# Kernel optimization log

Hardware: AMD Instinct MI355X
Metric: run time of the kernel (lower is better)

Reference implementation:

```python
import jax, jax.numpy as jnp
import numpy as np

P = 7      # local_patch_size
H = 6      # heads
DH = 30    # dim_head


def setup_inputs() -> dict:
    key = jax.random.key(0)
    ks = jax.random.split(key, 5)
    b, dim, L = 16, 180, 14336
    inner = H * DH  # 180
    fmap = jax.random.normal(ks[0], (b, dim, L), dtype=jnp.float32)
    Wq = jax.random.normal(ks[1], (inner, dim), dtype=jnp.float32) * 0.05
    Wkv = jax.random.normal(ks[2], (2 * inner, dim), dtype=jnp.float32) * 0.05
    Wo = jax.random.normal(ks[3], (dim, inner), dtype=jnp.float32) * 0.05
    bo = jax.random.normal(ks[4], (dim,), dtype=jnp.float32) * 0.05
    return {"fmap": fmap, "Wq": Wq, "Wkv": Wkv, "Wo": Wo, "bo": bo}


def reference(fmap, Wq, Wkv, Wo, bo):
    b, c, L = fmap.shape
    l = L // P
    scale = DH ** -0.5
    # 'b c (l p) -> b c l p' windows
    x = fmap.reshape(b, c, l, P)
    # pointwise (kernel-1) conv projections
    q = jnp.einsum('ec,bclp->belp', Wq, x)
    kv = jnp.einsum('ec,bclp->belp', Wkv, x)
    k, v = jnp.split(kv, 2, axis=1)

    def split_heads(t):
        # (b, h*d, l, p) -> (b, l, h, p, d)
        return t.reshape(b, H, DH, l, P).transpose(0, 3, 1, 4, 2)

    q, k, v = map(split_heads, (q, k, v))
    dots = jnp.einsum('blhid,blhjd->blhij', q, k) * scale  # per-window 7x7 scores
    attn = jax.nn.softmax(dots, axis=-1)
    out = jnp.einsum('blhij,blhjd->blhid', attn, v)  # (b, l, h, p, d)
    # '(b l h) p d -> b (h d) (l p)'
    out = out.transpose(0, 2, 4, 1, 3).reshape(b, H * DH, l * P)
    return jnp.einsum('oe,bel->bol', Wo, out) + bo[None, :, None]
```

## Files before the change

kernel.cpp:

```cpp
#include <hip/hip_runtime.h>
#include <stdint.h>

namespace {

constexpr int DIM  = 180;
constexpr int LL   = 14336;
constexpr int B    = 16;
constexpr int T    = 56;
constexpr int NCH  = 256;
constexpr int EQKV = 540;
constexpr int EPAD = 192;

constexpr int QT_STRIDE = 584;
constexpr int XS_STRIDE = 200;
constexpr int QT_U16  = T * QT_STRIDE;
constexpr int XS_U16  = 32 * XS_STRIDE;
constexpr int LDS_U16 = QT_U16 + XS_U16 + 544;

typedef __attribute__((ext_vector_type(8))) short bf16x8;
typedef __attribute__((ext_vector_type(4))) float f32x4;

union Frag { bf16x8 v; uint32_t u[4]; unsigned short s[8]; };

__device__ __forceinline__ unsigned short f2b(float f) {
  uint32_t u = __builtin_bit_cast(uint32_t, f);
  u = (u + 0x7fffu + ((u >> 16) & 1u)) >> 16;
  return (unsigned short)u;
}
__device__ __forceinline__ uint32_t pack2(float lo, float hi) {
  return (uint32_t)f2b(lo) | ((uint32_t)f2b(hi) << 16);
}
__device__ __forceinline__ float blo(uint32_t u) { return __builtin_bit_cast(float, u << 16); }
__device__ __forceinline__ float bhi(uint32_t u) { return __builtin_bit_cast(float, u & 0xffff0000u); }
__device__ __forceinline__ f32x4 zero4() { f32x4 z = {0.f,0.f,0.f,0.f}; return z; }
__device__ __forceinline__ bf16x8 zfrag() {
  Frag f; f.u[0]=f.u[1]=f.u[2]=f.u[3]=0u; return f.v;
}

}

__global__ __launch_bounds__(1024) void la_prep(
    const float* __restrict__ Wq, const float* __restrict__ Wkv,
    const float* __restrict__ Wo, unsigned short* __restrict__ wqkv_b,
    unsigned short* __restrict__ wo_b) {
  const int idx = (int)(blockIdx.x * 1024 + threadIdx.x);
  if (idx < EQKV * EPAD) {
    const int e = idx / EPAD, c = idx - e * EPAD;
    float v = 0.f;
    if (c < DIM) v = (e < DIM) ? Wq[e * DIM + c] : Wkv[(size_t)(e - DIM) * DIM + c];
    wqkv_b[idx] = f2b(v);
  } else {
    const int k = idx - EQKV * EPAD;
    if (k < DIM * EPAD) {
      const int o = k / EPAD, cc = k - o * EPAD;
      const int h = cc >> 5, d = cc & 31;
      float v = 0.f;
      if (d < 30) v = Wo[o * DIM + h * 30 + d];
      wo_b[k] = f2b(v);
    }
  }
}

__global__ __launch_bounds__(512, 4) void la_main(
    const float* __restrict__ fmap, const unsigned short* __restrict__ wqkv,
    const unsigned short* __restrict__ wo_b, const float* __restrict__ bo,
    float* __restrict__ out) {
  __shared__ unsigned short lds[LDS_U16];
  unsigned short* qt  = lds;
  unsigned short* xs  = lds + QT_U16;
  unsigned short* lut = xs + XS_U16;

  const int tid  = (int)threadIdx.x;
  const int wave = tid >> 6;
  const int lane = tid & 63;
  const int l15  = lane & 15;
  const int g    = lane >> 4;

  const int bi    = (int)blockIdx.x;
  const int b     = bi >> 8;
  const int chunk = bi & 255;
  const int t0    = chunk * T;

  for (int e = tid; e < EQKV; e += 512) {
    const int part = (e >= 360) ? 2 : ((e >= DIM) ? 1 : 0);
    const int rr = e - part * DIM;
    const int h = rr / 30;
    const int d = rr - h * 30;
    lut[e] = (unsigned short)(part * EPAD + h * 32 + d);
  }

#pragma unroll
  for (int ph = 0; ph < 2; ++ph) {
    const int tb = ph * 32;
    __syncthreads();
#pragma unroll
    for (int it = 0; it < 3; ++it) {
      const int idx = tid + it * 512;
      const int c  = idx >> 3;
      const int tl = (idx & 7) * 4;
      float4 v = {0.f, 0.f, 0.f, 0.f};
      if (c < DIM && (tb + tl) < T)
        v = *(const float4*)(fmap + (size_t)(b * DIM + c) * LL + t0 + tb + tl);
      unsigned short* xr = xs + tl * XS_STRIDE + c;
      xr[0 * XS_STRIDE] = f2b(v.x);
      xr[1 * XS_STRIDE] = f2b(v.y);
      xr[2 * XS_STRIDE] = f2b(v.z);
      xr[3 * XS_STRIDE] = f2b(v.w);
    }
    __syncthreads();
    for (int mt = wave; mt < 36; mt += 8) {
      const int e_a = mt * 16 + l15;
      f32x4 acc0 = zero4(), acc1 = zero4();
#pragma unroll
      for (int ks = 0; ks < 6; ++ks) {
        const int c0 = ks * 32 + g * 8;
        const bf16x8 a = (e_a < EQKV)
            ? *(const bf16x8*)(wqkv + (size_t)e_a * EPAD + c0) : zfrag();
        const bf16x8 b0 = *(const bf16x8*)(xs + l15 * XS_STRIDE + c0);
        const bf16x8 b1 = *(const bf16x8*)(xs + (16 + l15) * XS_STRIDE + c0);
        acc0 = __builtin_amdgcn_mfma_f32_16x16x32_bf16(a, b0, acc0, 0, 0, 0);
        acc1 = __builtin_amdgcn_mfma_f32_16x16x32_bf16(a, b1, acc1, 0, 0, 0);
      }
      const int e0 = mt * 16 + g * 4;
#pragma unroll
      for (int nt = 0; nt < 2; ++nt) {
        const f32x4 A = nt ? acc1 : acc0;
        const int t = tb + nt * 16 + l15;
        if (t < T) {
          unsigned short* qrow = qt + t * QT_STRIDE;
          if (e0 + 0 < EQKV) qrow[lut[e0 + 0]] = f2b(A[0]);
          if (e0 + 1 < EQKV) qrow[lut[e0 + 1]] = f2b(A[1]);
          if (e0 + 2 < EQKV) qrow[lut[e0 + 2]] = f2b(A[2]);
          if (e0 + 3 < EQKV) qrow[lut[e0 + 3]] = f2b(A[3]);
        }
      }
    }
  }
  __syncthreads();

  if (tid < 336) {
    const float scale = 0.18257418583505536f;
    const int w   = tid / 42;
    const int rem = tid - w * 42;
    const int h   = rem / 7;
    const int i   = rem - h * 7;
    const int ti  = w * 7 + i;
    const uint32_t* qrow = (const uint32_t*)(qt + ti * QT_STRIDE + h * 32);
    const unsigned short* kbase = qt + (w * 7) * QT_STRIDE + EPAD + h * 32;
    float dots[7];
#pragma unroll
    for (int j = 0; j < 7; ++j) dots[j] = 0.f;
#pragma unroll
    for (int dp = 0; dp < 15; ++dp) {
      const uint32_t qu = qrow[dp];
      const float q0 = blo(qu), q1 = bhi(qu);
#pragma unroll
      for (int j = 0; j < 7; ++j) {
        const uint32_t ku = *(const uint32_t*)(kbase + j * QT_STRIDE + dp * 2);
        dots[j] += q0 * blo(ku);
        dots[j] += q1 * bhi(ku);
      }
    }
    float mx = dots[0];
#pragma unroll
    for (int j = 1; j < 7; ++j) mx = fmaxf(mx, dots[j]);
    float aw[7];
    float s = 0.f;
#pragma unroll
    for (int j = 0; j < 7; ++j) {
      const float pj = __expf(scale * (dots[j] - mx));
      aw[j] = pj; s += pj;
    }
    const float inv = 1.f / s;
#pragma unroll
    for (int j = 0; j < 7; ++j) aw[j] *= inv;
    const unsigned short* vbase = qt + (w * 7) * QT_STRIDE + 2 * EPAD + h * 32;
    uint32_t* orow = (uint32_t*)(qt + ti * QT_STRIDE + h * 32);
#pragma unroll
    for (int dp = 0; dp < 15; ++dp) {
      float o0 = 0.f, o1 = 0.f;
#pragma unroll
      for (int j = 0; j < 7; ++j) {
        const uint32_t vu = *(const uint32_t*)(vbase + j * QT_STRIDE + dp * 2);
        o0 += aw[j] * blo(vu);
        o1 += aw[j] * bhi(vu);
      }
      orow[dp] = pack2(o0, o1);
    }
    orow[15] = 0u;
  }
  __syncthreads();

  for (int p = wave; p < 48; p += 8) {
    const int m = p >> 2;
    const int n = p & 3;
    const int o_a  = m * 16 + l15;
    const int tcol = n * 16 + l15;
    const int trd  = (tcol < T) ? tcol : (T - 1);
    f32x4 acc = zero4();
#pragma unroll
    for (int ks = 0; ks < 6; ++ks) {
      const int c0 = ks * 32 + g * 8;
      const bf16x8 a = (o_a < DIM)
          ? *(const bf16x8*)(wo_b + (size_t)o_a * EPAD + c0) : zfrag();
      const bf16x8 bf = *(const bf16x8*)(qt + trd * QT_STRIDE + c0);
      acc = __builtin_amdgcn_mfma_f32_16x16x32_bf16(a, bf, acc, 0, 0, 0);
    }
    if (tcol < T) {
#pragma unroll
      for (int r = 0; r < 4; ++r) {
        const int o = m * 16 + g * 4 + r;
        if (o < DIM)
          out[(size_t)(b * DIM + o) * LL + t0 + tcol] = acc[r] + bo[o];
      }
    }
  }
}

extern "C" void kernel_launch(void* const* d_in, const int* in_sizes, int n_in,
                              void* d_out, int out_size, void* d_ws, size_t ws_size,
                              hipStream_t stream) {
  const float* fmap = (const float*)d_in[0];
  const float* Wq   = (const float*)d_in[1];
  const float* Wkv  = (const float*)d_in[2];
  const float* Wo   = (const float*)d_in[3];
  const float* bo   = (const float*)d_in[4];
  float* o = (float*)d_out;

  unsigned short* wqkv_b = (unsigned short*)d_ws;
  unsigned short* wo_b   = wqkv_b + EQKV * EPAD;

  const int prep_elems = EQKV * EPAD + DIM * EPAD;
  hipLaunchKernelGGL(la_prep, dim3((prep_elems + 1023) / 1024), dim3(1024), 0,
                     stream, Wq, Wkv, Wo, wqkv_b, wo_b);
  hipLaunchKernelGGL(la_main, dim3(B * NCH), dim3(512), 0, stream,
                     fmap, wqkv_b, wo_b, bo, o);
}
```

Baseline: 401.3 us.

## Halve token tile and load activations straight into MFMA register fragments

The token tile per block drops from 56 to 28, which doubles the grid. Each lane now gathers its fmap column straight into bf16 MFMA B-fragments held in registers, so the LDS staging buffer, its extra barriers and the LUT are gone. The head/dim index is computed arithmetically instead. This shrinks LDS so more blocks fit per CU (launch bounds raised to 6), but the per-lane fmap reads are strided by a full row rather than coalesced float4 loads, and each weight matrix fragment is reused over only 28 tokens.

Result: slower. 576.5 us (+43.7%).

```diff
diff --git a/kernel.cpp b/kernel.cpp
--- a/kernel.cpp
+++ b/kernel.cpp
@@ -6,16 +6,12 @@
 constexpr int DIM  = 180;
 constexpr int LL   = 14336;
 constexpr int B    = 16;
-constexpr int T    = 56;
-constexpr int NCH  = 256;
+constexpr int T    = 28;
+constexpr int NCH  = 512;
 constexpr int EQKV = 540;
 constexpr int EPAD = 192;
 
 constexpr int QT_STRIDE = 584;
-constexpr int XS_STRIDE = 200;
-constexpr int QT_U16  = T * QT_STRIDE;
-constexpr int XS_U16  = 32 * XS_STRIDE;
-constexpr int LDS_U16 = QT_U16 + XS_U16 + 544;
 
 typedef __attribute__((ext_vector_type(8))) short bf16x8;
 typedef __attribute__((ext_vector_type(4))) float f32x4;
@@ -61,14 +57,11 @@
   }
 }
 
-__global__ __launch_bounds__(512, 4) void la_main(
+__global__ __launch_bounds__(512, 6) void la_main(
     const float* __restrict__ fmap, const unsigned short* __restrict__ wqkv,
     const unsigned short* __restrict__ wo_b, const float* __restrict__ bo,
     float* __restrict__ out) {
-  __shared__ unsigned short lds[LDS_U16];
-  unsigned short* qt  = lds;
-  unsigned short* xs  = lds + QT_U16;
-  unsigned short* lut = xs + XS_U16;
+  __shared__ __align__(16) unsigned short qt[T * QT_STRIDE];
 
   const int tid  = (int)threadIdx.x;
   const int wave = tid >> 6;
@@ -77,68 +70,61 @@
   const int g    = lane >> 4;
 
   const int bi    = (int)blockIdx.x;
-  const int b     = bi >> 8;
-  const int chunk = bi & 255;
+  const int b     = bi >> 9;
+  const int chunk = bi & 511;
   const int t0    = chunk * T;
 
-  for (int e = tid; e < EQKV; e += 512) {
-    const int part = (e >= 360) ? 2 : ((e >= DIM) ? 1 : 0);
-    const int rr = e - part * DIM;
-    const int h = rr / 30;
-    const int d = rr - h * 30;
-    lut[e] = (unsigned short)(part * EPAD + h * 32 + d);
-  }
-
-#pragma unroll
-  for (int ph = 0; ph < 2; ++ph) {
-    const int tb = ph * 32;
-    __syncthreads();
-#pragma unroll
-    for (int it = 0; it < 3; ++it) {
-      const int idx = tid + it * 512;
-      const int c  = idx >> 3;
-      const int tl = (idx & 7) * 4;
-      float4 v = {0.f, 0.f, 0.f, 0.f};
-      if (c < DIM && (tb + tl) < T)
-        v = *(const float4*)(fmap + (size_t)(b * DIM + c) * LL + t0 + tb + tl);
-      unsigned short* xr = xs + tl * XS_STRIDE + c;
-      xr[0 * XS_STRIDE] = f2b(v.x);
-      xr[1 * XS_STRIDE] = f2b(v.y);
-      xr[2 * XS_STRIDE] = f2b(v.z);
-      xr[3 * XS_STRIDE] = f2b(v.w);
-    }
-    __syncthreads();
-    for (int mt = wave; mt < 36; mt += 8) {
-      const int e_a = mt * 16 + l15;
-      f32x4 acc0 = zero4(), acc1 = zero4();
-#pragma unroll
-      for (int ks = 0; ks < 6; ++ks) {
-        const int c0 = ks * 32 + g * 8;
-        const bf16x8 a = (e_a < EQKV)
-            ? *(const bf16x8*)(wqkv + (size_t)e_a * EPAD + c0) : zfrag();
-        const bf16x8 b0 = *(const bf16x8*)(xs + l15 * XS_STRIDE + c0);
-        const bf16x8 b1 = *(const bf16x8*)(xs + (16 + l15) * XS_STRIDE + c0);
-        acc0 = __builtin_amdgcn_mfma_f32_16x16x32_bf16(a, b0, acc0, 0, 0, 0);
-        acc1 = __builtin_amdgcn_mfma_f32_16x16x32_bf16(a, b1, acc1, 0, 0, 0);
-      }
+  const int mq = wave >> 1;
+  const int n  = wave & 1;
+  const int tl = n * 16 + l15;
+  const bool tvalid = (tl < T);
+
+  Frag breg[6];
+  {
+    const float* xbase = fmap + (size_t)b * DIM * LL + t0 + tl;
+#pragma unroll
+    for (int ks = 0; ks < 6; ++ks) {
+#pragma unroll
+      for (int j = 0; j < 8; ++j) {
+        const int c = ks * 32 + g * 8 + j;
+        float v = 0.f;
+        if (tvalid && c < DIM) v = xbase[c * LL];
+        breg[ks].s[j] = f2b(v);
+      }
+    }
+  }
+
+#pragma unroll 3
+  for (int k9 = 0; k9 < 9; ++k9) {
+    const int mt  = mq * 9 + k9;
+    const int e_a = mt * 16 + l15;
+    f32x4 acc = zero4();
+#pragma unroll
+    for (int ks = 0; ks < 6; ++ks) {
+      const bf16x8 a = (e_a < EQKV)
+          ? *(const bf16x8*)(wqkv + (size_t)e_a * EPAD + ks * 32 + g * 8)
+          : zfrag();
+      acc = __builtin_amdgcn_mfma_f32_16x16x32_bf16(a, breg[ks].v, acc, 0, 0, 0);
+    }
+    if (tvalid) {
+      unsigned short* qrow = qt + tl * QT_STRIDE;
       const int e0 = mt * 16 + g * 4;
 #pragma unroll
-      for (int nt = 0; nt < 2; ++nt) {
-        const f32x4 A = nt ? acc1 : acc0;
-        const int t = tb + nt * 16 + l15;
-        if (t < T) {
-          unsigned short* qrow = qt + t * QT_STRIDE;
-          if (e0 + 0 < EQKV) qrow[lut[e0 + 0]] = f2b(A[0]);
-          if (e0 + 1 < EQKV) qrow[lut[e0 + 1]] = f2b(A[1]);
-          if (e0 + 2 < EQKV) qrow[lut[e0 + 2]] = f2b(A[2]);
-          if (e0 + 3 < EQKV) qrow[lut[e0 + 3]] = f2b(A[3]);
+      for (int r = 0; r < 4; ++r) {
+        const int e = e0 + r;
+        if (e < EQKV) {
+          const int part = (e >= 360) ? 2 : ((e >= DIM) ? 1 : 0);
+          const int rr = e - part * DIM;
+          const int h  = (rr * 34953) >> 20;
+          const int d  = rr - h * 30;
+          qrow[part * EPAD + h * 32 + d] = f2b(acc[r]);
         }
       }
     }
   }
   __syncthreads();
 
-  if (tid < 336) {
+  if (tid < 168) {
     const float scale = 0.18257418583505536f;
     const int w   = tid / 42;
     const int rem = tid - w * 42;
@@ -191,11 +177,11 @@
   }
   __syncthreads();
 
-  for (int p = wave; p < 48; p += 8) {
-    const int m = p >> 2;
-    const int n = p & 3;
+  for (int p = wave; p < 24; p += 8) {
+    const int m  = p >> 1;
+    const int n3 = p & 1;
     const int o_a  = m * 16 + l15;
-    const int tcol = n * 16 + l15;
+    const int tcol = n3 * 16 + l15;
     const int trd  = (tcol < T) ? tcol : (T - 1);
     f32x4 acc = zero4();
 #pragma unroll
```

## Split fused kernel into QKV GEMM and attention+out-proj kernels via workspace

Applied to the files above, without the earlier changes.

Replaces the single fused kernel with two kernels. The first computes the QKV projection for 64-token tiles with larger per-wave register tiles and writes bf16 QKV to a global workspace. The second reads that workspace, computes the per-window attention from registers and does the output projection on 112-token tiles. Batches are processed in groups sized to the available workspace, with the old fused kernel kept as a fallback. The aim is better MFMA operand reuse and less LDS pressure, paid for with an extra global round trip of the intermediate QKV tensor.

Result: slower. 1.253 ms (+212.2%).

```diff
diff --git a/kernel.cpp b/kernel.cpp
--- a/kernel.cpp
+++ b/kernel.cpp
@@ -6,14 +6,17 @@
 constexpr int DIM  = 180;
 constexpr int LL   = 14336;
 constexpr int B    = 16;
-constexpr int T    = 56;
-constexpr int NCH  = 256;
 constexpr int EQKV = 540;
 constexpr int EPAD = 192;
 
+constexpr int QROW = 544;
+constexpr int K1T  = 64;
+constexpr int K2T  = 112;
+
+constexpr int F_T = 56;
 constexpr int QT_STRIDE = 584;
 constexpr int XS_STRIDE = 200;
-constexpr int QT_U16  = T * QT_STRIDE;
+constexpr int QT_U16  = F_T * QT_STRIDE;
 constexpr int XS_U16  = 32 * XS_STRIDE;
 constexpr int LDS_U16 = QT_U16 + XS_U16 + 544;
 
@@ -42,26 +45,245 @@
 __global__ __launch_bounds__(1024) void la_prep(
     const float* __restrict__ Wq, const float* __restrict__ Wkv,
     const float* __restrict__ Wo, unsigned short* __restrict__ wqkv_b,
-    unsigned short* __restrict__ wo_b) {
+    unsigned short* __restrict__ wo_h32, unsigned short* __restrict__ wo_nat) {
   const int idx = (int)(blockIdx.x * 1024 + threadIdx.x);
-  if (idx < EQKV * EPAD) {
-    const int e = idx / EPAD, c = idx - e * EPAD;
+  if (idx < 576 * 192) {
+    const int e = idx / 192, c = idx - e * 192;
     float v = 0.f;
-    if (c < DIM) v = (e < DIM) ? Wq[e * DIM + c] : Wkv[(size_t)(e - DIM) * DIM + c];
+    if (e < EQKV && c < DIM)
+      v = (e < DIM) ? Wq[e * DIM + c] : Wkv[(size_t)(e - DIM) * DIM + c];
     wqkv_b[idx] = f2b(v);
+  } else if (idx < 576 * 192 + 192 * 192) {
+    const int k = idx - 576 * 192;
+    const int o = k / 192, cc = k - o * 192;
+    const int h = cc >> 5, d = cc & 31;
+    float v = 0.f;
+    if (o < DIM && d < 30) v = Wo[o * DIM + h * 30 + d];
+    wo_h32[k] = f2b(v);
   } else {
-    const int k = idx - EQKV * EPAD;
-    if (k < DIM * EPAD) {
-      const int o = k / EPAD, cc = k - o * EPAD;
-      const int h = cc >> 5, d = cc & 31;
-      float v = 0.f;
-      if (d < 30) v = Wo[o * DIM + h * 30 + d];
-      wo_b[k] = f2b(v);
-    }
-  }
-}
-
-__global__ __launch_bounds__(512, 4) void la_main(
+    const int k = idx - 576 * 192 - 192 * 192;
+    const int o = k / 192, c = k - o * 192;
+    float v = 0.f;
+    if (o < DIM && c < DIM) v = Wo[o * DIM + c];
+    wo_nat[k] = f2b(v);
+  }
+}
+
+__global__ __launch_bounds__(512, 4) void k1_qkv(
+    const float* __restrict__ fmap, const unsigned short* __restrict__ wqkv,
+    unsigned short* __restrict__ qkv, int b0) {
+  __shared__ __align__(16) unsigned short xs[K1T * 200];
+
+  const int tid  = (int)threadIdx.x;
+  const int wave = tid >> 6;
+  const int lane = tid & 63;
+  const int l15  = lane & 15;
+  const int g    = lane >> 4;
+
+  const int bl = (int)blockIdx.x / 224;
+  const int b  = b0 + bl;
+  const int t0 = ((int)blockIdx.x - bl * 224) * K1T;
+
+#pragma unroll
+  for (int it = 0; it < 6; ++it) {
+    const int idx = tid + it * 512;
+    const int c = idx >> 4;
+    const int t = (idx & 15) * 4;
+    float4 v = {0.f, 0.f, 0.f, 0.f};
+    if (c < DIM)
+      v = *(const float4*)(fmap + ((size_t)b * DIM + c) * LL + t0 + t);
+    xs[(t + 0) * 200 + c] = f2b(v.x);
+    xs[(t + 1) * 200 + c] = f2b(v.y);
+    xs[(t + 2) * 200 + c] = f2b(v.z);
+    xs[(t + 3) * 200 + c] = f2b(v.w);
+  }
+  __syncthreads();
+
+  const int nmt = (wave < 4) ? 5 : 4;
+  f32x4 acc[5][4];
+#pragma unroll
+  for (int i = 0; i < 5; ++i)
+#pragma unroll
+    for (int n = 0; n < 4; ++n) acc[i][n] = zero4();
+
+#pragma unroll
+  for (int ks = 0; ks < 6; ++ks) {
+    const int c0 = ks * 32 + g * 8;
+    bf16x8 bfr[4];
+#pragma unroll
+    for (int n = 0; n < 4; ++n)
+      bfr[n] = *(const bf16x8*)(xs + (n * 16 + l15) * 200 + c0);
+#pragma unroll
+    for (int i = 0; i < 5; ++i) {
+      if (i < nmt) {
+        const int e = (wave + i * 8) * 16 + l15;
+        const bf16x8 a = *(const bf16x8*)(wqkv + (size_t)e * EPAD + c0);
+#pragma unroll
+        for (int n = 0; n < 4; ++n)
+          acc[i][n] = __builtin_amdgcn_mfma_f32_16x16x32_bf16(a, bfr[n], acc[i][n], 0, 0, 0);
+      }
+    }
+  }
+
+  const size_t rowbase = (size_t)bl * LL + t0;
+#pragma unroll
+  for (int i = 0; i < 5; ++i) {
+    if (i < nmt) {
+      const int e0 = (wave + i * 8) * 16 + g * 4;
+      if (e0 < EQKV) {
+#pragma unroll
+        for (int n = 0; n < 4; ++n) {
+          const int t = n * 16 + l15;
+          uint2 pk;
+          pk.x = pack2(acc[i][n][0], acc[i][n][1]);
+          pk.y = pack2(acc[i][n][2], acc[i][n][3]);
+          *(uint2*)(qkv + (rowbase + t) * QROW + e0) = pk;
+        }
+      }
+    }
+  }
+}
+
+__global__ __launch_bounds__(512, 4) void k2_attn_oproj(
+    const unsigned short* __restrict__ qkv, const unsigned short* __restrict__ wo,
+    const float* __restrict__ bo, float* __restrict__ out, int b0) {
+  __shared__ __align__(16) unsigned short att[K2T * 200];
+
+  const int tid  = (int)threadIdx.x;
+  const int wave = tid >> 6;
+  const int lane = tid & 63;
+  const int l15  = lane & 15;
+  const int g    = lane >> 4;
+
+  const int bl = (int)blockIdx.x >> 7;
+  const int b  = b0 + bl;
+  const int t0 = ((int)blockIdx.x & 127) * K2T;
+  const size_t slbase = (size_t)bl * LL + t0;
+
+  if (tid < 384) {
+    const float scale = 0.18257418583505536f;
+    const int w   = tid / 24;
+    const int rem = tid - w * 24;
+    const int h   = rem >> 2;
+    const int p   = rem & 3;
+    const int i0  = 2 * p;
+    const bool two = (p < 3);
+    const size_t twb = slbase + w * 7;
+    const int hq = h * 30;
+
+    uint32_t q0[15], q1[15];
+    {
+      const uint32_t* qp0 = (const uint32_t*)(qkv + (twb + i0) * QROW + hq);
+      const uint32_t* qp1 = (const uint32_t*)(qkv + (twb + i0 + (two ? 1 : 0)) * QROW + hq);
+#pragma unroll
+      for (int dp = 0; dp < 15; ++dp) { q0[dp] = qp0[dp]; q1[dp] = qp1[dp]; }
+    }
+    float d0[7], d1[7];
+#pragma unroll
+    for (int j = 0; j < 7; ++j) {
+      const uint32_t* kp = (const uint32_t*)(qkv + (twb + j) * QROW + DIM + hq);
+      float s0 = 0.f, s1 = 0.f;
+#pragma unroll
+      for (int dp = 0; dp < 15; ++dp) {
+        const uint32_t ku = kp[dp];
+        const float kl = blo(ku), kh = bhi(ku);
+        s0 += blo(q0[dp]) * kl + bhi(q0[dp]) * kh;
+        s1 += blo(q1[dp]) * kl + bhi(q1[dp]) * kh;
+      }
+      d0[j] = s0; d1[j] = s1;
+    }
+    float aw0[7], aw1[7];
+    {
+      float mx0 = d0[0], mx1 = d1[0];
+#pragma unroll
+      for (int j = 1; j < 7; ++j) { mx0 = fmaxf(mx0, d0[j]); mx1 = fmaxf(mx1, d1[j]); }
+      float s0 = 0.f, s1 = 0.f;
+#pragma unroll
+      for (int j = 0; j < 7; ++j) {
+        aw0[j] = __expf(scale * (d0[j] - mx0)); s0 += aw0[j];
+        aw1[j] = __expf(scale * (d1[j] - mx1)); s1 += aw1[j];
+      }
+      const float r0 = 1.f / s0, r1 = 1.f / s1;
+#pragma unroll
+      for (int j = 0; j < 7; ++j) { aw0[j] *= r0; aw1[j] *= r1; }
+    }
+    float o0[30], o1[30];
+#pragma unroll
+    for (int d = 0; d < 30; ++d) { o0[d] = 0.f; o1[d] = 0.f; }
+#pragma unroll
+    for (int j = 0; j < 7; ++j) {
+      const uint32_t* vp = (const uint32_t*)(qkv + (twb + j) * QROW + 2 * DIM + hq);
+      const float a0 = aw0[j], a1 = aw1[j];
+#pragma unroll
+      for (int dp = 0; dp < 15; ++dp) {
+        const uint32_t vu = vp[dp];
+        const float vl = blo(vu), vh = bhi(vu);
+        o0[2 * dp]     += a0 * vl;  o0[2 * dp + 1] += a0 * vh;
+        o1[2 * dp]     += a1 * vl;  o1[2 * dp + 1] += a1 * vh;
+      }
+    }
+    unsigned short* ar0 = att + (w * 7 + i0) * 200 + hq;
+#pragma unroll
+    for (int dp = 0; dp < 15; ++dp)
+      *(uint32_t*)(ar0 + 2 * dp) = pack2(o0[2 * dp], o0[2 * dp + 1]);
+    if (two) {
+      unsigned short* ar1 = ar0 + 200;
+#pragma unroll
+      for (int dp = 0; dp < 15; ++dp)
+        *(uint32_t*)(ar1 + 2 * dp) = pack2(o1[2 * dp], o1[2 * dp + 1]);
+    }
+  }
+  for (int idx = tid; idx < K2T * 6; idx += 512) {
+    const int t = idx / 6;
+    const int j = idx - t * 6;
+    *(uint32_t*)(att + t * 200 + DIM + 2 * j) = 0u;
+  }
+  __syncthreads();
+
+  const int w_m = wave >> 1;
+  const int w_n = wave & 1;
+  const int ntb = w_n * 4;
+  const int nnt = w_n ? 3 : 4;
+  f32x4 acc[3][4];
+#pragma unroll
+  for (int i = 0; i < 3; ++i)
+#pragma unroll
+    for (int n = 0; n < 4; ++n) acc[i][n] = zero4();
+#pragma unroll
+  for (int ks = 0; ks < 6; ++ks) {
+    const int c0 = ks * 32 + g * 8;
+    bf16x8 bfr[4];
+#pragma unroll
+    for (int n = 0; n < 4; ++n)
+      if (n < nnt)
+        bfr[n] = *(const bf16x8*)(att + ((ntb + n) * 16 + l15) * 200 + c0);
+#pragma unroll
+    for (int i = 0; i < 3; ++i) {
+      const int o = (w_m * 3 + i) * 16 + l15;
+      const bf16x8 a = *(const bf16x8*)(wo + (size_t)o * EPAD + c0);
+#pragma unroll
+      for (int n = 0; n < 4; ++n)
+        if (n < nnt)
+          acc[i][n] = __builtin_amdgcn_mfma_f32_16x16x32_bf16(a, bfr[n], acc[i][n], 0, 0, 0);
+    }
+  }
+#pragma unroll
+  for (int i = 0; i < 3; ++i) {
+#pragma unroll
+    for (int r = 0; r < 4; ++r) {
+      const int o = (w_m * 3 + i) * 16 + g * 4 + r;
+      if (o < DIM) {
+        const float bias = bo[o];
+        float* orow = out + ((size_t)b * DIM + o) * LL + t0;
+#pragma unroll
+        for (int n = 0; n < 4; ++n)
+          if (n < nnt) orow[(ntb + n) * 16 + l15] = acc[i][n][r] + bias;
+      }
+    }
+  }
+}
+
+__global__ __launch_bounds__(512, 4) void la_fused(
     const float* __restrict__ fmap, const unsigned short* __restrict__ wqkv,
     const unsigned short* __restrict__ wo_b, const float* __restrict__ bo,
     float* __restrict__ out) {
@@ -79,7 +301,7 @@
   const int bi    = (int)blockIdx.x;
   const int b     = bi >> 8;
   const int chunk = bi & 255;
-  const int t0    = chunk * T;
+  const int t0    = chunk * F_T;
 
   for (int e = tid; e < EQKV; e += 512) {
     const int part = (e >= 360) ? 2 : ((e >= DIM) ? 1 : 0);
@@ -99,7 +321,7 @@
       const int c  = idx >> 3;
       const int tl = (idx & 7) * 4;
       float4 v = {0.f, 0.f, 0.f, 0.f};
-      if (c < DIM && (tb + tl) < T)
+      if (c < DIM && (tb + tl) < F_T)
         v = *(const float4*)(fmap + (size_t)(b * DIM + c) * LL + t0 + tb + tl);
       unsigned short* xr = xs + tl * XS_STRIDE + c;
       xr[0 * XS_STRIDE] = f2b(v.x);
@@ -126,7 +348,7 @@
       for (int nt = 0; nt < 2; ++nt) {
         const f32x4 A = nt ? acc1 : acc0;
         const int t = tb + nt * 16 + l15;
-        if (t < T) {
+        if (t < F_T) {
           unsigned short* qrow = qt + t * QT_STRIDE;
           if (e0 + 0 < EQKV) qrow[lut[e0 + 0]] = f2b(A[0]);
           if (e0 + 1 < EQKV) qrow[lut[e0 + 1]] = f2b(A[1]);
@@ -196,7 +418,7 @@
     const int n = p & 3;
     const int o_a  = m * 16 + l15;
     const int tcol = n * 16 + l15;
-    const int trd  = (tcol < T) ? tcol : (T - 1);
+    const int trd  = (tcol < F_T) ? tcol : (F_T - 1);
     f32x4 acc = zero4();
 #pragma unroll
     for (int ks = 0; ks < 6; ++ks) {
@@ -206,7 +428,7 @@
       const bf16x8 bf = *(const bf16x8*)(qt + trd * QT_STRIDE + c0);
       acc = __builtin_amdgcn_mfma_f32_16x16x32_bf16(a, bf, acc, 0, 0, 0);
     }
-    if (tcol < T) {
+    if (tcol < F_T) {
 #pragma unroll
       for (int r = 0; r < 4; ++r) {
         const int o = m * 16 + g * 4 + r;
@@ -228,11 +450,31 @@
   float* o = (float*)d_out;
 
   unsigned short* wqkv_b = (unsigned short*)d_ws;
-  unsigned short* wo_b   = wqkv_b + EQKV * EPAD;
-
-  const int prep_elems = EQKV * EPAD + DIM * EPAD;
-  hipLaunchKernelGGL(la_prep, dim3((prep_elems + 1023) / 1024), dim3(1024), 0,
-                     stream, Wq, Wkv, Wo, wqkv_b, wo_b);
-  hipLaunchKernelGGL(la_main, dim3(B * NCH), dim3(512), 0, stream,
-                     fmap, wqkv_b, wo_b, bo, o);
-}
+  unsigned short* wo_h32 = wqkv_b + 576 * 192;
+  unsigned short* wo_nat = wo_h32 + 192 * 192;
+  const size_t woff = (size_t)(576 * 192 + 2 * 192 * 192) * 2;
+
+  hipLaunchKernelGGL(la_prep, dim3(180), dim3(1024), 0, stream,
+                     Wq, Wkv, Wo, wqkv_b, wo_h32, wo_nat);
+
+  const size_t per_batch = (size_t)LL * QROW * 2;
+  int SB = 0;
+  if      (woff + 16 * per_batch <= ws_size) SB = 16;
+  else if (woff +  8 * per_batch <= ws_size) SB = 8;
+  else if (woff +  4 * per_batch <= ws_size) SB = 4;
+  else if (woff +  2 * per_batch <= ws_size) SB = 2;
+  else if (woff +  1 * per_batch <= ws_size) SB = 1;
+
+  if (SB > 0) {
+    unsigned short* qkv_ws = (unsigned short*)((char*)d_ws + woff);
+    for (int s = 0; s < B; s += SB) {
+      hipLaunchKernelGGL(k1_qkv, dim3(SB * 224), dim3(512), 0, stream,
+                         fmap, wqkv_b, qkv_ws, s);
+      hipLaunchKernelGGL(k2_attn_oproj, dim3(SB * 128), dim3(512), 0, stream,
+                         qkv_ws, wo_nat, bo, o, s);
+    }
+  } else {
+    hipLaunchKernelGGL(la_fused, dim3(4096), dim3(512), 0, stream,
+                       fmap, wqkv_b, wo_h32, bo, o);
+  }
+}
```
